# Kernel tuning notes

Hardware: AMD Instinct MI355X
Metric: run time of the kernel (lower is better)

Reference implementation:

```python
import jax, jax.numpy as jnp
import numpy as np
from jax import lax

EPS = 1e-5
K = 32  # k_neighbor

def conv1(x, w):
    # x: [B, Cin, L], w: [Cout, Cin] (1x1 conv, no bias)
    return jnp.einsum('bcl,oc->bol', x, w)

def bn(x, g, b):
    # BatchNorm1d in training mode: batch statistics over (batch, length)
    m = jnp.mean(x, axis=(0, 2), keepdims=True)
    v = jnp.var(x, axis=(0, 2), keepdims=True)
    return g[None, :, None] * (x - m) / jnp.sqrt(v + EPS) + b[None, :, None]

def res_block(x, w1, g1, b1, w2, g2, b2):
    h = jax.nn.gelu(bn(conv1(x, w1), g1, b1), approximate=False)
    h = bn(conv1(h, w2), g2, b2)
    return jax.nn.gelu(h + x, approximate=False)

def extraction(x, conv_w, bn_g, bn_b, fw, fg, fb):
    # conv_w: [n_blocks, 2, C, C]; bn_g/bn_b: [n_blocks, 2, C]
    for i in range(conv_w.shape[0]):
        x = res_block(x, conv_w[i, 0], bn_g[i, 0], bn_b[i, 0],
                      conv_w[i, 1], bn_g[i, 1], bn_b[i, 1])
    # TransformerBlock: ffn (conv+BN) with residual + GELU
    return jax.nn.gelu(x + bn(conv1(x, fw), fg, fb), approximate=False)

def setup_inputs() -> dict:
    key = jax.random.key(0)
    ks = jax.random.split(key, 16)
    B, N, S, C = 8, 4096, 1024, 128  # C = out_channel = 2*channel
    inp = {
        'xyz': jax.random.normal(ks[0], (B, N, 3), dtype=jnp.float32),
        'x': jax.random.normal(ks[1], (B, 64, N), dtype=jnp.float32),
        'fps_idx': jax.random.randint(ks[2], (B, S), 0, N, dtype=jnp.int64),
        'pre_conv_w': jax.random.normal(ks[3], (2, 2, C, C), dtype=jnp.float32) * 0.05,
        'pre_bn_g': jnp.ones((2, 2, C), jnp.float32),
        'pre_bn_b': jnp.zeros((2, 2, C), jnp.float32),
        'pre_ffn_w': jax.random.normal(ks[4], (C, C), dtype=jnp.float32) * 0.05,
        'pre_ffn_g': jnp.ones((C,), jnp.float32),
        'pre_ffn_b': jnp.zeros((C,), jnp.float32),
        'pos_conv_w': jax.random.normal(ks[5], (2, 2, C, C), dtype=jnp.float32) * 0.05,
        'pos_bn_g': jnp.ones((2, 2, C), jnp.float32),
        'pos_bn_b': jnp.zeros((2, 2, C), jnp.float32),
        'pos_ffn_w': jax.random.normal(ks[6], (C, C), dtype=jnp.float32) * 0.05,
        'pos_ffn_g': jnp.ones((C,), jnp.float32),
        'pos_ffn_b': jnp.zeros((C,), jnp.float32),
    }
    return inp

def reference(xyz, x, fps_idx,
              pre_conv_w, pre_bn_g, pre_bn_b, pre_ffn_w, pre_ffn_g, pre_ffn_b,
              pos_conv_w, pos_bn_g, pos_bn_b, pos_ffn_w, pos_ffn_g, pos_ffn_b):
    B, N, _ = xyz.shape
    S = fps_idx.shape[1]
    points = jnp.swapaxes(x, 1, 2)  # [B, N, d]
    d = points.shape[-1]

    # --- LocalGrouper ---
    new_xyz = jnp.take_along_axis(xyz, fps_idx[:, :, None], axis=1)      # [B, S, 3]
    new_pts = jnp.take_along_axis(points, fps_idx[:, :, None], axis=1)  # [B, S, d]

    # squared distances [B, S, N]
    sqr = (jnp.sum(new_xyz ** 2, -1)[:, :, None]
           + jnp.sum(xyz ** 2, -1)[:, None, :]
           - 2.0 * jnp.einsum('bsc,bnc->bsn', new_xyz, xyz))
    idx = lax.top_k(-sqr, K)[1]  # [B, S, K] smallest distances

    grouped = jnp.take_along_axis(points, idx.reshape(B, S * K)[:, :, None],
                                  axis=1).reshape(B, S, K, d)
    center = new_pts[:, :, None, :]  # [B, S, 1, d]
    feat = jnp.concatenate([grouped - center,
                            jnp.broadcast_to(center, grouped.shape)], axis=-1)  # [B,S,K,2d]

    C = 2 * d
    # --- PreExtraction: [B,S,K,C] -> [B*S, C, K] -> maxpool -> [B, C, S] ---
    y = jnp.swapaxes(feat, 2, 3).reshape(B * S, C, K)
    y = extraction(y, pre_conv_w, pre_bn_g, pre_bn_b, pre_ffn_w, pre_ffn_g, pre_ffn_b)
    y = jnp.max(y, axis=-1).reshape(B, S, C)
    y = jnp.swapaxes(y, 1, 2)  # [B, C, S]

    # --- PosExtraction ---
    y = extraction(y, pos_conv_w, pos_bn_g, pos_bn_b, pos_ffn_w, pos_ffn_g, pos_ffn_b)
    return (new_xyz, y)
```

## Files before the change

kernel.cpp:

```cpp
#include <hip/hip_runtime.h>
#include <math.h>

typedef unsigned short ushort_t;
typedef unsigned long long u64;
typedef unsigned int uint32;

#define B_ 8
#define N_ 4096
#define S_ 1024
#define K_ 32
#define C_ 128
#define NCOL1 (B_*S_*K_)
#define NCOL2 (B_*S_)
#define EPS_ 1e-5f

typedef ushort_t us8 __attribute__((ext_vector_type(8)));
typedef short s16x8 __attribute__((ext_vector_type(8)));
typedef float f32x4 __attribute__((ext_vector_type(4)));

__device__ __forceinline__ float bf2f(ushort_t u){ return __uint_as_float(((uint32)u)<<16); }
__device__ __forceinline__ ushort_t f2bf(float f){
    uint32 x = __float_as_uint(f);
    return (ushort_t)((x + 0x7FFFu + ((x>>16)&1u)) >> 16);
}
__device__ __forceinline__ float gelu_f(float v){
    float az = fabsf(v)*0.70710678118654752f;
    float t  = __builtin_amdgcn_rcpf(fmaf(0.3275911f, az, 1.0f));
    float p  = fmaf(fmaf(fmaf(fmaf(1.061405429f, t, -1.453152027f), t, 1.421413741f), t,
                   -0.284496736f), t, 0.254829592f)*t;
    float e  = __expf(-az*az);
    float er = fmaf(-p, e, 1.0f);
    float s  = (v < 0.0f) ? -er : er;
    return 0.5f*v*(1.0f+s);
}
__device__ __forceinline__ u64 shfl_xor_u64(u64 v, int m){
    int lo = __shfl_xor((int)(v & 0xFFFFFFFFull), m, 64);
    int hi = __shfl_xor((int)(v >> 32), m, 64);
    return (((u64)(uint32)hi) << 32) | (uint32)lo;
}
__device__ __forceinline__ void gl_lds16(const char* gp, char* lp){
    __builtin_amdgcn_global_load_lds((const __attribute__((address_space(1))) void*)gp,
                                     (__attribute__((address_space(3))) void*)lp, 16, 0, 0);
}

__global__ __launch_bounds__(256) void transpose_kernel(const float* __restrict__ x, ushort_t* __restrict__ xTb){
    __shared__ float t[64][65];
    int b  = blockIdx.x >> 6;
    int n0 = (blockIdx.x & 63) * 64;
    int tx = threadIdx.x & 63, ty = threadIdx.x >> 6;
    #pragma unroll
    for (int i=0;i<16;i++){
        int c = i*4 + ty;
        t[c][tx] = x[((long)(b*64 + c))*N_ + n0 + tx];
    }
    __syncthreads();
    #pragma unroll
    for (int i=0;i<16;i++){
        int n = i*4 + ty;
        xTb[((long)(b*N_ + n0 + n))*64 + tx] = f2bf(t[tx][n]);
    }
}

__global__ __launch_bounds__(256) void knn_kernel(const float* __restrict__ xyz, const int* __restrict__ fps,
                                                  int* __restrict__ idxg, float* __restrict__ newxyz){
    __shared__ uint32 hist[4096];
    __shared__ u64    cand[1024];
    __shared__ u64    out_keys[64];
    __shared__ uint32 csum[256];
    __shared__ uint32 wtot[4];
    __shared__ uint32 shv[8];
    __shared__ u64    wred[4];
    __shared__ u64    winner;

    int tid = threadIdx.x;
    int wv = tid >> 6, l = tid & 63;
    int bs = blockIdx.x;
    int b  = bs >> 10;
    int qi = fps[bs];
    const float* qb = xyz + ((long)b*N_ + qi)*3;
    float qx = qb[0], qy = qb[1], qz = qb[2];
    if (tid < 3) newxyz[(long)bs*3 + tid] = qb[tid];
    const float* xb = xyz + (long)b*N_*3;

    for (int i=tid;i<1024;i+=256) hist[i]=0;
    if (tid < 8) shv[tid]=0;
    __syncthreads();

    uint32 dbits[16];
    #pragma unroll
    for (int i=0;i<16;i++){
        int n = i*256 + tid;
        float dx = xb[n*3+0]-qx, dy = xb[n*3+1]-qy, dz = xb[n*3+2]-qz;
        float d = dx*dx + dy*dy + dz*dz;
        dbits[i] = __float_as_uint(d);
        atomicAdd(&hist[dbits[i]>>21], 1u);
    }
    __syncthreads();

    {
        uint32 h4[4]; uint32 csumv=0;
        #pragma unroll
        for (int i=0;i<4;i++){ h4[i]=hist[tid*4+i]; csumv+=h4[i]; }
        uint32 sc = csumv;
        #pragma unroll
        for (int off=1; off<64; off<<=1){ uint32 o=__shfl_up(sc,off,64); if (l>=off) sc+=o; }
        if (l==63) wtot[wv]=sc;
        csum[tid]=sc;
        __syncthreads();
        uint32 base=0;
        for (int w2=0; w2<wv; w2++) base += wtot[w2];
        uint32 cum = base + csum[tid] - csumv;
        #pragma unroll
        for (int i=0;i<4;i++){
            if (cum <= 31u && 31u < cum + h4[i]){ shv[0]=(uint32)(tid*4+i); shv[1]=cum; }
            cum += h4[i];
        }
    }
    __syncthreads();
    uint32 b1 = shv[0], cl1 = shv[1];

    for (int i=tid;i<4096;i+=256) hist[i]=0;
    __syncthreads();
    #pragma unroll
    for (int i=0;i<16;i++){
        uint32 u = dbits[i];
        if ((u>>21)==b1) atomicAdd(&hist[(u>>9)&0xFFFu], 1u);
    }
    __syncthreads();

    uint32 r2 = 31u - cl1;
    {
        uint32 h[16]; uint32 csumv=0;
        #pragma unroll
        for (int i=0;i<16;i++){ h[i]=hist[tid*16+i]; csumv += h[i]; }
        uint32 sc = csumv;
        #pragma unroll
        for (int off=1; off<64; off<<=1){ uint32 o=__shfl_up(sc,off,64); if (l>=off) sc+=o; }
        if (l==63) wtot[wv]=sc;
        csum[tid]=sc;
        __syncthreads();
        uint32 base=0;
        for (int w2=0; w2<wv; w2++) base += wtot[w2];
        uint32 cum = base + csum[tid] - csumv;
        #pragma unroll
        for (int i=0;i<16;i++){
            if (cum <= r2 && r2 < cum + h[i]){ shv[2]=(uint32)(tid*16+i); shv[3]=cum; }
            cum += h[i];
        }
    }
    __syncthreads();
    uint32 b2 = shv[2], cl2 = shv[3];
    uint32 nless = cl1 + cl2;

    #pragma unroll
    for (int i=0;i<16;i++){
        uint32 u = dbits[i];
        int n = i*256 + tid;
        uint32 bb1 = u >> 21;
        if (bb1 > b1) continue;
        u64 key = (((u64)u)<<32) | (uint32)n;
        if (bb1 < b1){
            uint32 p = atomicAdd(&shv[4],1u); out_keys[p] = key;
        } else {
            uint32 bb2 = (u>>9)&0xFFFu;
            if (bb2 < b2){ uint32 p = atomicAdd(&shv[4],1u); out_keys[p] = key; }
            else if (bb2 == b2){ uint32 p = atomicAdd(&shv[5],1u); if (p < 1024u) cand[p] = key; }
        }
    }
    __syncthreads();

    if (shv[5] > 1024u){
        uint32 alive = 0xFFFFu;
        for (int r=0;r<K_;r++){
            u64 lmin = ~0ull;
            #pragma unroll
            for (int i=0;i<16;i++){
                u64 k = (((u64)dbits[i])<<32) | (uint32)(i*256+tid);
                if (((alive>>i)&1u) && k < lmin) lmin = k;
            }
            #pragma unroll
            for (int off=32; off>=1; off>>=1){
                u64 o = shfl_xor_u64(lmin, off);
                if (o < lmin) lmin = o;
            }
            if (l == 0) wred[wv] = lmin;
            __syncthreads();
            if (tid == 0){
                u64 m = wred[0];
                if (wred[1]<m) m=wred[1];
                if (wred[2]<m) m=wred[2];
                if (wred[3]<m) m=wred[3];
                winner = m;
                idxg[(long)bs*K_ + r] = (int)(m & 0xFFFFFFFFull);
            }
            __syncthreads();
            u64 w = winner;
            #pragma unroll
            for (int i=0;i<16;i++){
                u64 k = (((u64)dbits[i])<<32) | (uint32)(i*256+tid);
                if (k == w) alive &= ~(1u<<i);
            }
        }
    } else if (wv == 0){
        uint32 cb   = shv[5];
        uint32 need = 32u - nless;
        for (uint32 r=0; r<need; r++){
            u64 lmin = ~0ull;
            for (uint32 s=l; s<cb; s+=64){ u64 kk = cand[s]; if (kk < lmin) lmin = kk; }
            #pragma unroll
            for (int off=32; off>=1; off>>=1){
                u64 o = shfl_xor_u64(lmin, off);
                if (o < lmin) lmin = o;
            }
            for (uint32 s=l; s<cb; s+=64){ if (cand[s]==lmin) cand[s] = ~0ull; }
            if (l==0) out_keys[nless + r] = lmin;
        }
        u64 key = (l < 32) ? out_keys[l] : ~0ull;
        #pragma unroll
        for (uint32 k=2; k<=64; k<<=1){
            bool dir = ((l & k)==0);
            #pragma unroll
            for (uint32 j=k>>1; j>=1; j>>=1){
                u64 o = shfl_xor_u64(key, j);
                bool lower = ((l & j)==0);
                u64 mn = (key < o) ? key : o;
                u64 mx = (key < o) ? o : key;
                key = (lower == dir) ? mn : mx;
            }
        }
        if (l < 32) idxg[(long)bs*K_ + l] = (int)(key & 0xFFFFFFFFull);
    }
}

__global__ __launch_bounds__(256) void wcvt_kernel(const float* __restrict__ pcw, const float* __restrict__ pfw,
                                                   const float* __restrict__ qcw, const float* __restrict__ qfw,
                                                   ushort_t* __restrict__ Wb, ushort_t* __restrict__ UW,
                                                   ushort_t* __restrict__ VW){
    int i = blockIdx.x*256 + threadIdx.x;
    if (i < 163840){
        int mat = i >> 14;
        int r = i & 16383;
        float v;
        if (mat < 4)       v = pcw[i];
        else if (mat == 4) v = pfw[r];
        else if (mat < 9)  v = qcw[i - 5*16384];
        else               v = qfw[r];
        Wb[i] = f2bf(v);
    } else {
        int j = i - 163840;
        int jj = j & 8191;
        int oc = jj >> 6, c = jj & 63;
        if (j < 8192) UW[jj] = f2bf(pcw[oc*128 + c]);
        else          VW[jj] = f2bf(pcw[oc*128 + 64 + c] - pcw[oc*128 + c]);
    }
}

__global__ __launch_bounds__(256) void uv_gemm(const ushort_t* __restrict__ xTb, const int* __restrict__ fps,
                                               const ushort_t* __restrict__ UW, const ushort_t* __restrict__ VW,
                                               ushort_t* __restrict__ U, ushort_t* __restrict__ V2){
    int tid = threadIdx.x;
    int w = tid >> 6, l = tid & 63;
    int l15 = l & 15, l4 = l >> 4;
    bool isV = blockIdx.x >= 256;
    int base = (isV ? (int)(blockIdx.x - 256) : (int)blockIdx.x)*128 + w*32;
    const ushort_t* Wh = isV ? VW : UW;
    ushort_t* out = isV ? V2 : U;

    long xrow[2];
    #pragma unroll
    for (int n=0;n<2;n++){
        int r = base + n*16 + l15;
        if (isV){ int b = r >> 10; xrow[n] = ((long)(b<<12) + fps[r]); }
        else    { xrow[n] = r; }
    }
    f32x4 acc[8][2] = {};
    #pragma unroll
    for (int ks=0; ks<2; ks++){
        int kl = ks*32 + l4*8;
        s16x8 af[8];
        #pragma unroll
        for (int m=0;m<8;m++)
            af[m] = *(const s16x8*)(Wh + (m*16 + l15)*64 + kl);
        s16x8 bv[2];
        #pragma unroll
        for (int n=0;n<2;n++)
            bv[n] = *(const s16x8*)(xTb + xrow[n]*64 + kl);
        #pragma unroll
        for (int m=0;m<8;m++)
            #pragma unroll
            for (int n=0;n<2;n++)
                acc[m][n] = __builtin_amdgcn_mfma_f32_16x16x32_bf16(af[m], bv[n], acc[m][n], 0, 0, 0);
    }
    #pragma unroll
    for (int n=0;n<2;n++){
        long radr = (long)(base + n*16 + l15)*C_;
        #pragma unroll
        for (int m=0;m<8;m++){
            f32x4 a = acc[m][n];
            uint2 st;
            st.x = (((uint32)f2bf(a[1]))<<16) | f2bf(a[0]);
            st.y = (((uint32)f2bf(a[3]))<<16) | f2bf(a[2]);
            *(uint2*)(out + radr + m*16 + l4*4) = st;
        }
    }
}

template<int MODE>
__global__ __launch_bounds__(256) void conv_mfma(const ushort_t* in1, const ushort_t* in2, ushort_t* aux,
                                                 ushort_t* out, const ushort_t* __restrict__ Wb,
                                                 const float* __restrict__ scsh_g,
                                                 const ushort_t* __restrict__ U, const ushort_t* __restrict__ V2,
                                                 const ushort_t* __restrict__ xTb, const int* __restrict__ idxg,
                                                 const int* __restrict__ fps,
                                                 float* __restrict__ pb, int nb, float inv_cnt){
    __shared__ ushort_t inT[16384];
    __shared__ float ss[256];
    __shared__ float sL[4][128], qL[4][128];
    int tid = threadIdx.x;
    int w = tid >> 6, l = tid & 63;
    int l15 = l & 15, l4 = l >> 4;
    long col0 = ((long)blockIdx.x << 7) + ((long)w << 5);

    if (MODE != 3){
        const char* gt = (const char*)(in1 + (((long)blockIdx.x) << 7)*C_);
        char* lb = (char*)inT;
        #pragma unroll
        for (int i=0;i<8;i++){
            int p = i*4096 + w*1024 + l*16;
            int src = p ^ (((p>>8)&7)<<4);
            gl_lds16(gt + src, lb + i*4096 + w*1024);
        }
    }

    s16x8 a2[8];
    if (MODE == 2){
        #pragma unroll
        for (int t=0;t<8;t++){
            int n = t>>2, ks = t&3;
            a2[t] = *(const s16x8*)(in2 + (col0 + n*16 + l15)*C_ + ks*32 + l4*8);
        }
    }
    if (MODE == 4){
        int bs = (int)(col0 >> 5);
        int b  = bs >> 10;
        int cc = fps[bs];
        const ushort_t* crow = xTb + ((long)(b<<12) + cc)*64;
        s16x8 c0 = *(const s16x8*)(crow + l4*8);
        s16x8 c1 = *(const s16x8*)(crow + 32 + l4*8);
        #pragma unroll
        for (int n=0;n<2;n++){
            int nn = idxg[col0 + n*16 + l15];
            const ushort_t* prow = xTb + ((long)(b<<12) + nn)*64;
            s16x8 p0 = *(const s16x8*)(prow + l4*8);
            s16x8 p1 = *(const s16x8*)(prow + 32 + l4*8);
            s16x8 d0, d1;
            #pragma unroll
            for (int e=0;e<8;e++){
                d0[e] = (short)f2bf(bf2f((ushort_t)p0[e]) - bf2f((ushort_t)c0[e]));
                d1[e] = (short)f2bf(bf2f((ushort_t)p1[e]) - bf2f((ushort_t)c1[e]));
            }
            a2[n*4+0] = d0; a2[n*4+1] = d1; a2[n*4+2] = c0; a2[n*4+3] = c1;
        }
    }
    if (MODE == 1 || MODE == 2 || MODE == 4) ss[tid] = scsh_g[tid];
    __syncthreads();

    f32x4 acc[8][2] = {};
    if (MODE == 3){
        int bs = (int)(col0 >> 5);
        int b  = bs >> 10;
        const ushort_t* vrow = V2 + (long)bs*C_;
        #pragma unroll
        for (int n=0;n<2;n++){
            int nn = idxg[col0 + n*16 + l15];
            const ushort_t* urow = U + ((long)(b*4096) + nn)*C_;
            #pragma unroll
            for (int m=0;m<8;m++){
                int oc0 = m*16 + l4*4;
                uint2 uu = *(const uint2*)(urow + oc0);
                uint2 vv = *(const uint2*)(vrow + oc0);
                acc[m][n][0] = bf2f((ushort_t)(uu.x & 0xFFFFu)) + bf2f((ushort_t)(vv.x & 0xFFFFu));
                acc[m][n][1] = bf2f((ushort_t)(uu.x >> 16))     + bf2f((ushort_t)(vv.x >> 16));
                acc[m][n][2] = bf2f((ushort_t)(uu.y & 0xFFFFu)) + bf2f((ushort_t)(vv.y & 0xFFFFu));
                acc[m][n][3] = bf2f((ushort_t)(uu.y >> 16))     + bf2f((ushort_t)(vv.y >> 16));
            }
        }
    } else {
        char* lb = (char*)inT;
        #pragma unroll
        for (int ks=0; ks<4; ks++){
            int kl = ks*32 + l4*8;
            s16x8 af[8];
            #pragma unroll
            for (int m=0;m<8;m++)
                af[m] = *(const s16x8*)(Wb + (m*16 + l15)*C_ + kl);
            s16x8 bv[2];
            int qsv[2];
            #pragma unroll
            for (int n=0;n<2;n++){
                int q = (w*32 + n*16 + l15)*256 + ks*64 + l4*16;
                qsv[n] = q ^ (((q>>8)&7)<<4);
                bv[n] = *(const s16x8*)(lb + qsv[n]);
            }
            if (MODE != 0){
                float sc[8], sh[8];
                const float4* sp = (const float4*)(&ss[kl*2]);
                float4 s0 = sp[0], s1 = sp[1], s2 = sp[2], s3 = sp[3];
                sc[0]=s0.x; sh[0]=s0.y; sc[1]=s0.z; sh[1]=s0.w;
                sc[2]=s1.x; sh[2]=s1.y; sc[3]=s1.z; sh[3]=s1.w;
                sc[4]=s2.x; sh[4]=s2.y; sc[5]=s2.z; sh[5]=s2.w;
                sc[6]=s3.x; sh[6]=s3.y; sc[7]=s3.z; sh[7]=s3.w;
                #pragma unroll
                for (int n=0;n<2;n++){
                    s16x8 v = bv[n];
                    if (MODE == 1){
                        #pragma unroll
                        for (int e=0;e<8;e++){
                            float f = gelu_f(fmaf(bf2f((ushort_t)v[e]), sc[e], sh[e]));
                            v[e] = (short)f2bf(f);
                        }
                    } else {
                        s16x8 a = a2[n*4+ks];
                        #pragma unroll
                        for (int e=0;e<8;e++){
                            float f = gelu_f(fmaf(bf2f((ushort_t)v[e]), sc[e], sh[e]) + bf2f((ushort_t)a[e]));
                            v[e] = (short)f2bf(f);
                        }
                    }
                    bv[n] = v;
                    if (MODE == 2 || MODE == 4)
                        *(s16x8*)(lb + qsv[n]) = v;
                }
            }
            #pragma unroll
            for (int m=0;m<8;m++)
                #pragma unroll
                for (int n=0;n<2;n++)
                    acc[m][n] = __builtin_amdgcn_mfma_f32_16x16x32_bf16(af[m], bv[n], acc[m][n], 0, 0, 0);
        }
    }

    if (MODE == 2 || MODE == 4){
        __syncthreads();
        char* auxb = (char*)aux + ((long)blockIdx.x << 15);
        const char* lb = (const char*)inT;
        #pragma unroll
        for (int i=0;i<8;i++){
            int lin = i*4096 + tid*16;
            int qs = lin ^ (((lin>>8)&7)<<4);
            *(f32x4*)(auxb + lin) = *(const f32x4*)(lb + qs);
        }
        __syncthreads();
    }

    {
        char* lb = (char*)inT;
        #pragma unroll
        for (int n=0;n<2;n++){
            #pragma unroll
            for (int m=0;m<8;m++){
                f32x4 a = acc[m][n];
                uint2 st;
                st.x = (((uint32)f2bf(a[1]))<<16) | f2bf(a[0]);
                st.y = (((uint32)f2bf(a[3]))<<16) | f2bf(a[2]);
                int q = (w*32 + n*16 + l15)*256 + (m*16 + l4*4)*2;
                int qs = q ^ (((q>>8)&7)<<4);
                *(uint2*)(lb + qs) = st;
            }
        }
        __syncthreads();
        char* outb = (char*)out + ((long)blockIdx.x << 15);
        const char* lb2 = (const char*)inT;
        #pragma unroll
        for (int i=0;i<8;i++){
            int lin = i*4096 + tid*16;
            int qs = lin ^ (((lin>>8)&7)<<4);
            *(f32x4*)(outb + lin) = *(const f32x4*)(lb2 + qs);
        }
    }

    #pragma unroll
    for (int m=0;m<8;m++){
        #pragma unroll
        for (int r=0;r<4;r++){
            float a0=acc[m][0][r], a1=acc[m][1][r];
            float s = a0+a1;
            float q = a0*a0+a1*a1;
            #pragma unroll
            for (int off=1; off<16; off<<=1){
                s += __shfl_xor(s, off, 64);
                q += __shfl_xor(q, off, 64);
            }
            if (l15 == 0){
                sL[w][m*16 + l4*4 + r] = s;
                qL[w][m*16 + l4*4 + r] = q;
            }
        }
    }
    __syncthreads();
    if (tid < 128){
        float s = sL[0][tid] + sL[1][tid] + sL[2][tid] + sL[3][tid];
        float q = qL[0][tid] + qL[1][tid] + qL[2][tid] + qL[3][tid];
        pb[(long)tid*nb + blockIdx.x]       = s;
        pb[(long)(128+tid)*nb + blockIdx.x] = q;
    }
}

__global__ __launch_bounds__(256) void reduce_fin_kernel(const float* __restrict__ pb, float* __restrict__ scsh,
                                                         const float* __restrict__ g, const float* __restrict__ bb,
                                                         float inv_cnt, int nb){
    int oc = blockIdx.x;
    float s=0.f, q=0.f;
    for (int b=threadIdx.x; b<nb; b+=256){
        s += pb[(long)oc*nb + b];
        q += pb[(long)(128+oc)*nb + b];
    }
    __shared__ float ls[256], lq[256];
    ls[threadIdx.x]=s; lq[threadIdx.x]=q;
    __syncthreads();
    #pragma unroll
    for (int st_=128; st_>0; st_>>=1){
        if (threadIdx.x < st_){ ls[threadIdx.x]+=ls[threadIdx.x+st_]; lq[threadIdx.x]+=lq[threadIdx.x+st_]; }
        __syncthreads();
    }
    if (threadIdx.x==0){
        float mean = ls[0]*inv_cnt;
        float var  = lq[0]*inv_cnt - mean*mean;
        float sc   = g[oc]*rsqrtf(var + EPS_);
        scsh[oc*2+0] = sc;
        scsh[oc*2+1] = bb[oc] - mean*sc;
    }
}

__global__ __launch_bounds__(256) void pool_kernel(const ushort_t* __restrict__ T, const ushort_t* __restrict__ X,
                                                   const float* __restrict__ scsh, ushort_t* __restrict__ A2){
    long p  = (long)blockIdx.x*256 + threadIdx.x;
    long bs = p >> 6;
    int  c0 = ((int)p & 63)*2;
    float sc0=scsh[c0*2], sh0=scsh[c0*2+1], sc1=scsh[c0*2+2], sh1=scsh[c0*2+3];
    const ushort_t* tb = T + (bs*K_)*(long)C_ + c0;
    const ushort_t* xv = X + (bs*K_)*(long)C_ + c0;
    float m0 = -1e30f, m1 = -1e30f;
    #pragma unroll 4
    for (int k=0;k<K_;k++){
        uint32 tv = *(const uint32*)(tb + (long)k*C_);
        uint32 av = *(const uint32*)(xv + (long)k*C_);
        float v0 = gelu_f(fmaf(bf2f((ushort_t)(tv & 0xFFFFu)), sc0, sh0) + bf2f((ushort_t)(av & 0xFFFFu)));
        float v1 = gelu_f(fmaf(bf2f((ushort_t)(tv >> 16)),     sc1, sh1) + bf2f((ushort_t)(av >> 16)));
        m0 = fmaxf(m0, v0);
        m1 = fmaxf(m1, v1);
    }
    uint32 o = (((uint32)f2bf(m1))<<16) | f2bf(m0);
    *(uint32*)(A2 + bs*C_ + c0) = o;
}

__global__ __launch_bounds__(256) void out2_kernel(const ushort_t* __restrict__ T, const ushort_t* __restrict__ X,
                                                   const float* __restrict__ scsh_g, float* __restrict__ y){
    __shared__ ushort_t Ts[16384];
    __shared__ ushort_t Xs[16384];
    __shared__ float ss[256];
    int tid = threadIdx.x, w = tid>>6, l = tid&63;
    int blk = blockIdx.x;

    {
        const char* gt = (const char*)(T + ((long)blk << 7)*C_);
        const char* gx = (const char*)(X + ((long)blk << 7)*C_);
        #pragma unroll
        for (int i=0;i<8;i++){
            int p = i*4096 + w*1024 + l*16;
            int src = p ^ (((p>>8)&7)<<4);
            gl_lds16(gt + src, (char*)Ts + i*4096 + w*1024);
            gl_lds16(gx + src, (char*)Xs + i*4096 + w*1024);
        }
    }
    ss[tid] = scsh_g[tid];
    __syncthreads();

    int b  = blk >> 3;
    int s0 = (blk & 7) * 128;
    int colL = tid & 127;
    int rep  = tid >> 7;
    #pragma unroll
    for (int cb=0; cb<8; cb++){
        int q  = colL*256 + rep*128 + cb*16;
        int qs = q ^ (((q>>8)&7)<<4);
        s16x8 tvv = *(const s16x8*)((char*)Ts + qs);
        s16x8 xvv = *(const s16x8*)((char*)Xs + qs);
        #pragma unroll
        for (int e=0;e<8;e++){
            int c = rep*64 + cb*8 + e;
            float f = gelu_f(fmaf(bf2f((ushort_t)tvv[e]), ss[c*2], ss[c*2+1]) + bf2f((ushort_t)xvv[e]));
            y[((long)(b*C_ + c))*S_ + s0 + colL] = f;
        }
    }
}

extern "C" void kernel_launch(void* const* d_in, const int* in_sizes, int n_in,
                              void* d_out, int out_size, void* d_ws, size_t ws_size,
                              hipStream_t stream){
    const float* xyz        = (const float*)d_in[0];
    const float* x          = (const float*)d_in[1];
    const int*   fps        = (const int*)d_in[2];
    const float* pre_conv_w = (const float*)d_in[3];
    const float* pre_bn_g   = (const float*)d_in[4];
    const float* pre_bn_b   = (const float*)d_in[5];
    const float* pre_ffn_w  = (const float*)d_in[6];
    const float* pre_ffn_g  = (const float*)d_in[7];
    const float* pre_ffn_b  = (const float*)d_in[8];
    const float* pos_conv_w = (const float*)d_in[9];
    const float* pos_bn_g   = (const float*)d_in[10];
    const float* pos_bn_b   = (const float*)d_in[11];
    const float* pos_ffn_w  = (const float*)d_in[12];
    const float* pos_ffn_g  = (const float*)d_in[13];
    const float* pos_ffn_b  = (const float*)d_in[14];

    float* out_xyz = (float*)d_out;
    float* out_y   = (float*)d_out + (long)B_*S_*3;

    char* ws = (char*)d_ws;
    float*    scsh = (float*)(ws + 0);
    float*    pbE  = (float*)(ws + 10240);
    ushort_t* Wb   = (ushort_t*)(ws + 337920);
    ushort_t* UW   = (ushort_t*)(ws + 665600);
    ushort_t* VW   = (ushort_t*)(ws + 681984);
    int*      idx  = (int*)(ws + 698368);
    ushort_t* xTb  = (ushort_t*)(ws + 1746944);
    ushort_t* A2   = (ushort_t*)(ws + 5941248);
    float*    pb1  = (float*)(ws + 8038400);
    ushort_t* C2   = (ushort_t*)(ws + 8038400);
    ushort_t* Cb   = (ushort_t*)(ws + 10135552);
    ushort_t* X    = (ushort_t*)(ws + 77244416);
    ushort_t* U    = (ushort_t*)(ws + 77244416);
    ushort_t* V2   = (ushort_t*)(ws + 85633024);
    (void)in_sizes; (void)n_in; (void)out_size; (void)ws_size;

    const float inv1 = 1.0f/(float)NCOL1, inv2 = 1.0f/(float)NCOL2;
    const ushort_t* Wp = Wb;
    const ushort_t* Wq = Wb + 5*C_*C_;
    const int nb = 2048;

    wcvt_kernel<<<704,256,0,stream>>>(pre_conv_w, pre_ffn_w, pos_conv_w, pos_ffn_w, Wb, UW, VW);
    transpose_kernel<<<B_*(N_/64),256,0,stream>>>(x, xTb);
    knn_kernel<<<B_*S_,256,0,stream>>>(xyz, fps, idx, out_xyz);
    uv_gemm<<<320,256,0,stream>>>(xTb, fps, UW, VW, U, V2);

    {
        const float* G[5]  = {pre_bn_g, pre_bn_g+C_, pre_bn_g+2*C_, pre_bn_g+3*C_, pre_ffn_g};
        const float* Bv[5] = {pre_bn_b, pre_bn_b+C_, pre_bn_b+2*C_, pre_bn_b+3*C_, pre_ffn_b};
        conv_mfma<3><<<nb,256,0,stream>>>(nullptr, nullptr, nullptr, Cb, nullptr, nullptr,
                                          U, V2, nullptr, idx, fps, pb1, nb, inv1);
        reduce_fin_kernel<<<128,256,0,stream>>>(pb1, scsh+0*256, G[0], Bv[0], inv1, nb);
        conv_mfma<1><<<nb,256,0,stream>>>(Cb, nullptr, nullptr, Cb, Wp+1*C_*C_, scsh+0*256,
                                          nullptr, nullptr, nullptr, nullptr, nullptr, pb1, nb, inv1);
        reduce_fin_kernel<<<128,256,0,stream>>>(pb1, scsh+1*256, G[1], Bv[1], inv1, nb);
        conv_mfma<4><<<nb,256,0,stream>>>(Cb, nullptr, X, Cb, Wp+2*C_*C_, scsh+1*256,
                                          nullptr, nullptr, xTb, idx, fps, pb1, nb, inv1);
        reduce_fin_kernel<<<128,256,0,stream>>>(pb1, scsh+2*256, G[2], Bv[2], inv1, nb);
        conv_mfma<1><<<nb,256,0,stream>>>(Cb, nullptr, nullptr, Cb, Wp+3*C_*C_, scsh+2*256,
                                          nullptr, nullptr, nullptr, nullptr, nullptr, pb1, nb, inv1);
        reduce_fin_kernel<<<128,256,0,stream>>>(pb1, scsh+3*256, G[3], Bv[3], inv1, nb);
        conv_mfma<2><<<nb,256,0,stream>>>(Cb, X, X, Cb, Wp+4*C_*C_, scsh+3*256,
                                          nullptr, nullptr, nullptr, nullptr, nullptr, pb1, nb, inv1);
        reduce_fin_kernel<<<128,256,0,stream>>>(pb1, scsh+4*256, G[4], Bv[4], inv1, nb);
        pool_kernel<<<(NCOL2*64)/256,256,0,stream>>>(Cb, X, scsh+4*256, A2);
    }

    {
        const float* G[5]  = {pos_bn_g, pos_bn_g+C_, pos_bn_g+2*C_, pos_bn_g+3*C_, pos_ffn_g};
        const float* Bv[5] = {pos_bn_b, pos_bn_b+C_, pos_bn_b+2*C_, pos_bn_b+3*C_, pos_ffn_b};
        const int nb2 = 64;
        conv_mfma<0><<<nb2,256,0,stream>>>(A2, nullptr, nullptr, C2, Wq+0*C_*C_, nullptr,
                                           nullptr, nullptr, nullptr, nullptr, nullptr, pbE, nb2, inv2);
        reduce_fin_kernel<<<128,256,0,stream>>>(pbE, scsh+5*256, G[0], Bv[0], inv2, nb2);
        conv_mfma<1><<<nb2,256,0,stream>>>(C2, nullptr, nullptr, C2, Wq+1*C_*C_, scsh+5*256,
                                           nullptr, nullptr, nullptr, nullptr, nullptr, pbE, nb2, inv2);
        reduce_fin_kernel<<<128,256,0,stream>>>(pbE, scsh+6*256, G[1], Bv[1], inv2, nb2);
        conv_mfma<2><<<nb2,256,0,stream>>>(C2, A2, A2, C2, Wq+2*C_*C_, scsh+6*256,
                                           nullptr, nullptr, nullptr, nullptr, nullptr, pbE, nb2, inv2);
        reduce_fin_kernel<<<128,256,0,stream>>>(pbE, scsh+7*256, G[2], Bv[2], inv2, nb2);
        conv_mfma<1><<<nb2,256,0,stream>>>(C2, nullptr, nullptr, C2, Wq+3*C_*C_, scsh+7*256,
                                           nullptr, nullptr, nullptr, nullptr, nullptr, pbE, nb2, inv2);
        reduce_fin_kernel<<<128,256,0,stream>>>(pbE, scsh+8*256, G[3], Bv[3], inv2, nb2);
        conv_mfma<2><<<nb2,256,0,stream>>>(C2, A2, A2, C2, Wq+4*C_*C_, scsh+8*256,
                                           nullptr, nullptr, nullptr, nullptr, nullptr, pbE, nb2, inv2);
        reduce_fin_kernel<<<128,256,0,stream>>>(pbE, scsh+9*256, G[4], Bv[4], inv2, nb2);
        out2_kernel<<<64,256,0,stream>>>(C2, A2, scsh+9*256, out_y);
    }
}
```

Before: 583.5 us.

## Double-buffer conv tiles with async LDS prefetch and split gather-add kernel

Replaces the monolithic conv_mfma with conv_pipe. Each block now processes two 64-column tiles, prefetching the next tile into a second LDS buffer through global_load_lds while the current tile runs its MFMAs. Outputs and aux residuals are written straight from registers to global memory, dropping the LDS staging round-trip and its extra barriers, and BN stats are accumulated across tiles. The MODE 3 gather-add path moves into its own gadd_kernel. The trade-off is less parallelism per tile (16 columns per wave), scattered uint2 global stores, and a hard vmcnt(0) wait that may limit overlap.

```diff
diff --git a/kernel.cpp b/kernel.cpp
--- a/kernel.cpp
+++ b/kernel.cpp
@@ -14,7 +14,6 @@
 #define NCOL2 (B_*S_)
 #define EPS_ 1e-5f
 
-typedef ushort_t us8 __attribute__((ext_vector_type(8)));
 typedef short s16x8 __attribute__((ext_vector_type(8)));
 typedef float f32x4 __attribute__((ext_vector_type(4)));
 
@@ -42,6 +41,9 @@
     __builtin_amdgcn_global_load_lds((const __attribute__((address_space(1))) void*)gp,
                                      (__attribute__((address_space(3))) void*)lp, 16, 0, 0);
 }
+#define PIN_VMCNT0() do{ __builtin_amdgcn_sched_barrier(0); \
+                         asm volatile("s_waitcnt vmcnt(0)" ::: "memory"); \
+                         __builtin_amdgcn_sched_barrier(0); }while(0)
 
 __global__ __launch_bounds__(256) void transpose_kernel(const float* __restrict__ x, ushort_t* __restrict__ xTb){
     __shared__ float t[64][65];
@@ -305,88 +307,172 @@
     }
 }
 
-template<int MODE>
-__global__ __launch_bounds__(256) void conv_mfma(const ushort_t* in1, const ushort_t* in2, ushort_t* aux,
-                                                 ushort_t* out, const ushort_t* __restrict__ Wb,
-                                                 const float* __restrict__ scsh_g,
-                                                 const ushort_t* __restrict__ U, const ushort_t* __restrict__ V2,
-                                                 const ushort_t* __restrict__ xTb, const int* __restrict__ idxg,
-                                                 const int* __restrict__ fps,
-                                                 float* __restrict__ pb, int nb, float inv_cnt){
-    __shared__ ushort_t inT[16384];
+__global__ __launch_bounds__(256) void gadd_kernel(const ushort_t* __restrict__ U, const ushort_t* __restrict__ V2,
+                                                   const int* __restrict__ idxg, ushort_t* __restrict__ out,
+                                                   float* __restrict__ pb, int nb){
+    __shared__ float sL[4][128], qL[4][128];
+    int tid = threadIdx.x;
+    int w = tid >> 6, l = tid & 63;
+    int l15 = l & 15, l4 = l >> 4;
+    long col0 = ((long)blockIdx.x << 7) + ((long)w << 5);
+    int bs = (int)(col0 >> 5);
+    int b  = bs >> 10;
+    const ushort_t* vrow = V2 + (long)bs*C_;
+
+    f32x4 acc[8][2];
+    #pragma unroll
+    for (int n=0;n<2;n++){
+        int nn = idxg[col0 + n*16 + l15];
+        const ushort_t* urow = U + ((long)(b*4096) + nn)*C_;
+        #pragma unroll
+        for (int m=0;m<8;m++){
+            int oc0 = m*16 + l4*4;
+            uint2 uu = *(const uint2*)(urow + oc0);
+            uint2 vv = *(const uint2*)(vrow + oc0);
+            acc[m][n][0] = bf2f((ushort_t)(uu.x & 0xFFFFu)) + bf2f((ushort_t)(vv.x & 0xFFFFu));
+            acc[m][n][1] = bf2f((ushort_t)(uu.x >> 16))     + bf2f((ushort_t)(vv.x >> 16));
+            acc[m][n][2] = bf2f((ushort_t)(uu.y & 0xFFFFu)) + bf2f((ushort_t)(vv.y & 0xFFFFu));
+            acc[m][n][3] = bf2f((ushort_t)(uu.y >> 16))     + bf2f((ushort_t)(vv.y >> 16));
+        }
+    }
+    #pragma unroll
+    for (int n=0;n<2;n++){
+        long cadr = (col0 + n*16 + l15)*C_;
+        #pragma unroll
+        for (int m=0;m<8;m++){
+            f32x4 a = acc[m][n];
+            uint2 st;
+            st.x = (((uint32)f2bf(a[1]))<<16) | f2bf(a[0]);
+            st.y = (((uint32)f2bf(a[3]))<<16) | f2bf(a[2]);
+            *(uint2*)(out + cadr + m*16 + l4*4) = st;
+        }
+    }
+    #pragma unroll
+    for (int m=0;m<8;m++){
+        #pragma unroll
+        for (int r=0;r<4;r++){
+            float a0=acc[m][0][r], a1=acc[m][1][r];
+            float s = a0+a1;
+            float q = a0*a0+a1*a1;
+            #pragma unroll
+            for (int off=1; off<16; off<<=1){
+                s += __shfl_xor(s, off, 64);
+                q += __shfl_xor(q, off, 64);
+            }
+            if (l15 == 0){
+                sL[w][m*16 + l4*4 + r] = s;
+                qL[w][m*16 + l4*4 + r] = q;
+            }
+        }
+    }
+    __syncthreads();
+    if (tid < 128){
+        float s = sL[0][tid] + sL[1][tid] + sL[2][tid] + sL[3][tid];
+        float q = qL[0][tid] + qL[1][tid] + qL[2][tid] + qL[3][tid];
+        pb[(long)tid*nb + blockIdx.x]       = s;
+        pb[(long)(128+tid)*nb + blockIdx.x] = q;
+    }
+}
+
+template<int MODE, int NT>
+__global__ __launch_bounds__(256, 4) void conv_pipe(const ushort_t* in1, const ushort_t* in2, ushort_t* aux,
+        ushort_t* out, const ushort_t* __restrict__ Wb, const float* __restrict__ scsh_g,
+        const ushort_t* __restrict__ xTb, const int* __restrict__ idxg, const int* __restrict__ fps,
+        float* __restrict__ pb, int nb){
+    __shared__ ushort_t inT[2][8192];
     __shared__ float ss[256];
     __shared__ float sL[4][128], qL[4][128];
     int tid = threadIdx.x;
     int w = tid >> 6, l = tid & 63;
     int l15 = l & 15, l4 = l >> 4;
-    long col0 = ((long)blockIdx.x << 7) + ((long)w << 5);
-
-    if (MODE != 3){
-        const char* gt = (const char*)(in1 + (((long)blockIdx.x) << 7)*C_);
-        char* lb = (char*)inT;
-        #pragma unroll
-        for (int i=0;i<8;i++){
-            int p = i*4096 + w*1024 + l*16;
+    int G = gridDim.x;
+
+    sL[w][l] = 0.f; sL[w][64+l] = 0.f;
+    qL[w][l] = 0.f; qL[w][64+l] = 0.f;
+
+    {
+        const char* gt = (const char*)in1 + ((long)blockIdx.x << 14);
+        #pragma unroll
+        for (int i=0;i<4;i++){
+            int p = (w<<12) + (i<<10) + (l<<4);
             int src = p ^ (((p>>8)&7)<<4);
-            gl_lds16(gt + src, lb + i*4096 + w*1024);
-        }
-    }
-
-    s16x8 a2[8];
+            gl_lds16(gt + src, (char*)&inT[0][0] + (w<<12) + (i<<10));
+        }
+    }
+    s16x8 a2cur[4], a2nxt[4];
     if (MODE == 2){
-        #pragma unroll
-        for (int t=0;t<8;t++){
-            int n = t>>2, ks = t&3;
-            a2[t] = *(const s16x8*)(in2 + (col0 + n*16 + l15)*C_ + ks*32 + l4*8);
-        }
+        long c0 = ((long)blockIdx.x << 6) + (w<<4);
+        #pragma unroll
+        for (int ks=0;ks<4;ks++)
+            a2cur[ks] = *(const s16x8*)(in2 + (c0 + l15)*C_ + ks*32 + l4*8);
     }
     if (MODE == 4){
-        int bs = (int)(col0 >> 5);
+        long c0 = ((long)blockIdx.x << 6) + (w<<4);
+        int bs = (int)(c0 >> 5);
         int b  = bs >> 10;
         int cc = fps[bs];
         const ushort_t* crow = xTb + ((long)(b<<12) + cc)*64;
-        s16x8 c0 = *(const s16x8*)(crow + l4*8);
-        s16x8 c1 = *(const s16x8*)(crow + 32 + l4*8);
-        #pragma unroll
-        for (int n=0;n<2;n++){
-            int nn = idxg[col0 + n*16 + l15];
-            const ushort_t* prow = xTb + ((long)(b<<12) + nn)*64;
-            s16x8 p0 = *(const s16x8*)(prow + l4*8);
-            s16x8 p1 = *(const s16x8*)(prow + 32 + l4*8);
-            s16x8 d0, d1;
-            #pragma unroll
-            for (int e=0;e<8;e++){
-                d0[e] = (short)f2bf(bf2f((ushort_t)p0[e]) - bf2f((ushort_t)c0[e]));
-                d1[e] = (short)f2bf(bf2f((ushort_t)p1[e]) - bf2f((ushort_t)c1[e]));
-            }
-            a2[n*4+0] = d0; a2[n*4+1] = d1; a2[n*4+2] = c0; a2[n*4+3] = c1;
-        }
-    }
-    if (MODE == 1 || MODE == 2 || MODE == 4) ss[tid] = scsh_g[tid];
-    __syncthreads();
-
-    f32x4 acc[8][2] = {};
-    if (MODE == 3){
-        int bs = (int)(col0 >> 5);
-        int b  = bs >> 10;
-        const ushort_t* vrow = V2 + (long)bs*C_;
-        #pragma unroll
-        for (int n=0;n<2;n++){
-            int nn = idxg[col0 + n*16 + l15];
-            const ushort_t* urow = U + ((long)(b*4096) + nn)*C_;
-            #pragma unroll
-            for (int m=0;m<8;m++){
-                int oc0 = m*16 + l4*4;
-                uint2 uu = *(const uint2*)(urow + oc0);
-                uint2 vv = *(const uint2*)(vrow + oc0);
-                acc[m][n][0] = bf2f((ushort_t)(uu.x & 0xFFFFu)) + bf2f((ushort_t)(vv.x & 0xFFFFu));
-                acc[m][n][1] = bf2f((ushort_t)(uu.x >> 16))     + bf2f((ushort_t)(vv.x >> 16));
-                acc[m][n][2] = bf2f((ushort_t)(uu.y & 0xFFFFu)) + bf2f((ushort_t)(vv.y & 0xFFFFu));
-                acc[m][n][3] = bf2f((ushort_t)(uu.y >> 16))     + bf2f((ushort_t)(vv.y >> 16));
-            }
-        }
-    } else {
-        char* lb = (char*)inT;
+        s16x8 cv0 = *(const s16x8*)(crow + l4*8);
+        s16x8 cv1 = *(const s16x8*)(crow + 32 + l4*8);
+        int nn = idxg[c0 + l15];
+        const ushort_t* prow = xTb + ((long)(b<<12) + nn)*64;
+        s16x8 p0 = *(const s16x8*)(prow + l4*8);
+        s16x8 p1 = *(const s16x8*)(prow + 32 + l4*8);
+        s16x8 d0, d1;
+        #pragma unroll
+        for (int e=0;e<8;e++){
+            d0[e] = (short)f2bf(bf2f((ushort_t)p0[e]) - bf2f((ushort_t)cv0[e]));
+            d1[e] = (short)f2bf(bf2f((ushort_t)p1[e]) - bf2f((ushort_t)cv1[e]));
+        }
+        a2cur[0]=d0; a2cur[1]=d1; a2cur[2]=cv0; a2cur[3]=cv1;
+    }
+    if (MODE != 0) ss[tid] = scsh_g[tid];
+    __syncthreads();
+
+    #pragma unroll
+    for (int t=0; t<NT; t++){
+        long tile = (long)t*G + blockIdx.x;
+        long col0 = (tile << 6) + (w<<4);
+
+        if (t+1 < NT){
+            long tn = tile + G;
+            const char* gt = (const char*)in1 + (tn << 14);
+            #pragma unroll
+            for (int i=0;i<4;i++){
+                int p = (w<<12) + (i<<10) + (l<<4);
+                int src = p ^ (((p>>8)&7)<<4);
+                gl_lds16(gt + src, (char*)&inT[(t+1)&1][0] + (w<<12) + (i<<10));
+            }
+            if (MODE == 2){
+                long c1 = (tn << 6) + (w<<4);
+                #pragma unroll
+                for (int ks=0;ks<4;ks++)
+                    a2nxt[ks] = *(const s16x8*)(in2 + (c1 + l15)*C_ + ks*32 + l4*8);
+            }
+            if (MODE == 4){
+                long c1 = (tn << 6) + (w<<4);
+                int bs = (int)(c1 >> 5);
+                int b  = bs >> 10;
+                int cc = fps[bs];
+                const ushort_t* crow = xTb + ((long)(b<<12) + cc)*64;
+                s16x8 cv0 = *(const s16x8*)(crow + l4*8);
+                s16x8 cv1 = *(const s16x8*)(crow + 32 + l4*8);
+                int nn = idxg[c1 + l15];
+                const ushort_t* prow = xTb + ((long)(b<<12) + nn)*64;
+                s16x8 p0 = *(const s16x8*)(prow + l4*8);
+                s16x8 p1 = *(const s16x8*)(prow + 32 + l4*8);
+                s16x8 d0, d1;
+                #pragma unroll
+                for (int e=0;e<8;e++){
+                    d0[e] = (short)f2bf(bf2f((ushort_t)p0[e]) - bf2f((ushort_t)cv0[e]));
+                    d1[e] = (short)f2bf(bf2f((ushort_t)p1[e]) - bf2f((ushort_t)cv1[e]));
+                }
+                a2nxt[0]=d0; a2nxt[1]=d1; a2nxt[2]=cv0; a2nxt[3]=cv1;
+            }
+        }
+
+        const char* lb = (const char*)&inT[t&1][0];
+        f32x4 acc[8] = {};
         #pragma unroll
         for (int ks=0; ks<4; ks++){
             int kl = ks*32 + l4*8;
@@ -394,14 +480,9 @@
             #pragma unroll
             for (int m=0;m<8;m++)
                 af[m] = *(const s16x8*)(Wb + (m*16 + l15)*C_ + kl);
-            s16x8 bv[2];
-            int qsv[2];
-            #pragma unroll
-            for (int n=0;n<2;n++){
-                int q = (w*32 + n*16 + l15)*256 + ks*64 + l4*16;
-                qsv[n] = q ^ (((q>>8)&7)<<4);
-                bv[n] = *(const s16x8*)(lb + qsv[n]);
-            }
+            int q  = ((w<<4) + l15)*256 + ks*64 + (l4<<4);
+            int qs = q ^ (((q>>8)&7)<<4);
+            s16x8 v = *(const s16x8*)(lb + qs);
             if (MODE != 0){
                 float sc[8], sh[8];
                 const float4* sp = (const float4*)(&ss[kl*2]);
@@ -410,93 +491,67 @@
                 sc[2]=s1.x; sh[2]=s1.y; sc[3]=s1.z; sh[3]=s1.w;
                 sc[4]=s2.x; sh[4]=s2.y; sc[5]=s2.z; sh[5]=s2.w;
                 sc[6]=s3.x; sh[6]=s3.y; sc[7]=s3.z; sh[7]=s3.w;
-                #pragma unroll
-                for (int n=0;n<2;n++){
-                    s16x8 v = bv[n];
-                    if (MODE == 1){
-                        #pragma unroll
-                        for (int e=0;e<8;e++){
-                            float f = gelu_f(fmaf(bf2f((ushort_t)v[e]), sc[e], sh[e]));
-                            v[e] = (short)f2bf(f);
-                        }
-                    } else {
-                        s16x8 a = a2[n*4+ks];
-                        #pragma unroll
-                        for (int e=0;e<8;e++){
-                            float f = gelu_f(fmaf(bf2f((ushort_t)v[e]), sc[e], sh[e]) + bf2f((ushort_t)a[e]));
-                            v[e] = (short)f2bf(f);
-                        }
+                if (MODE == 1){
+                    #pragma unroll
+                    for (int e=0;e<8;e++){
+                        float f = gelu_f(fmaf(bf2f((ushort_t)v[e]), sc[e], sh[e]));
+                        v[e] = (short)f2bf(f);
                     }
-                    bv[n] = v;
-                    if (MODE == 2 || MODE == 4)
-                        *(s16x8*)(lb + qsv[n]) = v;
+                } else {
+                    s16x8 a = a2cur[ks];
+                    #pragma unroll
+                    for (int e=0;e<8;e++){
+                        float f = gelu_f(fmaf(bf2f((ushort_t)v[e]), sc[e], sh[e]) + bf2f((ushort_t)a[e]));
+                        v[e] = (short)f2bf(f);
+                    }
                 }
+                if (MODE == 2 || MODE == 4)
+                    *(s16x8*)(aux + (col0 + l15)*C_ + kl) = v;
             }
             #pragma unroll
             for (int m=0;m<8;m++)
-                #pragma unroll
-                for (int n=0;n<2;n++)
-                    acc[m][n] = __builtin_amdgcn_mfma_f32_16x16x32_bf16(af[m], bv[n], acc[m][n], 0, 0, 0);
-        }
-    }
-
-    if (MODE == 2 || MODE == 4){
-        __syncthreads();
-        char* auxb = (char*)aux + ((long)blockIdx.x << 15);
-        const char* lb = (const char*)inT;
-        #pragma unroll
-        for (int i=0;i<8;i++){
-            int lin = i*4096 + tid*16;
-            int qs = lin ^ (((lin>>8)&7)<<4);
-            *(f32x4*)(auxb + lin) = *(const f32x4*)(lb + qs);
-        }
-        __syncthreads();
-    }
-
-    {
-        char* lb = (char*)inT;
-        #pragma unroll
-        for (int n=0;n<2;n++){
+                acc[m] = __builtin_amdgcn_mfma_f32_16x16x32_bf16(af[m], v, acc[m], 0, 0, 0);
+        }
+
+        {
+            long cadr = (col0 + l15)*C_;
             #pragma unroll
             for (int m=0;m<8;m++){
-                f32x4 a = acc[m][n];
+                f32x4 a = acc[m];
                 uint2 st;
                 st.x = (((uint32)f2bf(a[1]))<<16) | f2bf(a[0]);
                 st.y = (((uint32)f2bf(a[3]))<<16) | f2bf(a[2]);
-                int q = (w*32 + n*16 + l15)*256 + (m*16 + l4*4)*2;
-                int qs = q ^ (((q>>8)&7)<<4);
-                *(uint2*)(lb + qs) = st;
-            }
-        }
-        __syncthreads();
-        char* outb = (char*)out + ((long)blockIdx.x << 15);
-        const char* lb2 = (const char*)inT;
-        #pragma unroll
-        for (int i=0;i<8;i++){
-            int lin = i*4096 + tid*16;
-            int qs = lin ^ (((lin>>8)&7)<<4);
-            *(f32x4*)(outb + lin) = *(const f32x4*)(lb2 + qs);
-        }
-    }
-
-    #pragma unroll
-    for (int m=0;m<8;m++){
-        #pragma unroll
-        for (int r=0;r<4;r++){
-            float a0=acc[m][0][r], a1=acc[m][1][r];
-            float s = a0+a1;
-            float q = a0*a0+a1*a1;
-            #pragma unroll
-            for (int off=1; off<16; off<<=1){
-                s += __shfl_xor(s, off, 64);
-                q += __shfl_xor(q, off, 64);
-            }
-            if (l15 == 0){
-                sL[w][m*16 + l4*4 + r] = s;
-                qL[w][m*16 + l4*4 + r] = q;
-            }
-        }
-    }
+                *(uint2*)(out + cadr + m*16 + l4*4) = st;
+            }
+        }
+
+        #pragma unroll
+        for (int m=0;m<8;m++){
+            #pragma unroll
+            for (int r=0;r<4;r++){
+                float s = acc[m][r];
+                float q = s*s;
+                #pragma unroll
+                for (int off=1; off<16; off<<=1){
+                    s += __shfl_xor(s, off, 64);
+                    q += __shfl_xor(q, off, 64);
+                }
+                if (l15 == 0){
+                    sL[w][m*16 + l4*4 + r] += s;
+                    qL[w][m*16 + l4*4 + r] += q;
+                }
+            }
+        }
+
+        if (t+1 < NT){
+            PIN_VMCNT0();
+            if (MODE == 2 || MODE == 4){
+                #pragma unroll
+                for (int ks=0;ks<4;ks++) a2cur[ks] = a2nxt[ks];
+            }
+        }
+    }
+
     __syncthreads();
     if (tid < 128){
         float s = sL[0][tid] + sL[1][tid] + sL[2][tid] + sL[3][tid];
@@ -601,16 +656,12 @@
     const float* xyz        = (const float*)d_in[0];
     const float* x          = (const float*)d_in[1];
     const int*   fps        = (const int*)d_in[2];
-    const float* pre_conv_w = (const float*)d_in[3];
     const float* pre_bn_g   = (const float*)d_in[4];
     const float* pre_bn_b   = (const float*)d_in[5];
-    const float* pre_ffn_w  = (const float*)d_in[6];
     const float* pre_ffn_g  = (const float*)d_in[7];
     const float* pre_ffn_b  = (const float*)d_in[8];
-    const float* pos_conv_w = (const float*)d_in[9];
     const float* pos_bn_g   = (const float*)d_in[10];
     const float* pos_bn_b   = (const float*)d_in[11];
-    const float* pos_ffn_w  = (const float*)d_in[12];
     const float* pos_ffn_g  = (const float*)d_in[13];
     const float* pos_ffn_b  = (const float*)d_in[14];
 
@@ -637,9 +688,11 @@
     const float inv1 = 1.0f/(float)NCOL1, inv2 = 1.0f/(float)NCOL2;
     const ushort_t* Wp = Wb;
     const ushort_t* Wq = Wb + 5*C_*C_;
-    const int nb = 2048;
-
-    wcvt_kernel<<<704,256,0,stream>>>(pre_conv_w, pre_ffn_w, pos_conv_w, pos_ffn_w, Wb, UW, VW);
+    const int G1 = 2048;
+    const int G2 = 64;
+
+    wcvt_kernel<<<704,256,0,stream>>>((const float*)d_in[3], (const float*)d_in[6],
+                                      (const float*)d_in[9], (const float*)d_in[12], Wb, UW, VW);
     transpose_kernel<<<B_*(N_/64),256,0,stream>>>(x, xTb);
     knn_kernel<<<B_*S_,256,0,stream>>>(xyz, fps, idx, out_xyz);
     uv_gemm<<<320,256,0,stream>>>(xTb, fps, UW, VW, U, V2);
@@ -647,43 +700,41 @@
     {
         const float* G[5]  = {pre_bn_g, pre_bn_g+C_, pre_bn_g+2*C_, pre_bn_g+3*C_, pre_ffn_g};
         const float* Bv[5] = {pre_bn_b, pre_bn_b+C_, pre_bn_b+2*C_, pre_bn_b+3*C_, pre_ffn_b};
-        conv_mfma<3><<<nb,256,0,stream>>>(nullptr, nullptr, nullptr, Cb, nullptr, nullptr,
-                                          U, V2, nullptr, idx, fps, pb1, nb, inv1);
-        reduce_fin_kernel<<<128,256,0,stream>>>(pb1, scsh+0*256, G[0], Bv[0], inv1, nb);
-        conv_mfma<1><<<nb,256,0,stream>>>(Cb, nullptr, nullptr, Cb, Wp+1*C_*C_, scsh+0*256,
-                                          nullptr, nullptr, nullptr, nullptr, nullptr, pb1, nb, inv1);
-        reduce_fin_kernel<<<128,256,0,stream>>>(pb1, scsh+1*256, G[1], Bv[1], inv1, nb);
-        conv_mfma<4><<<nb,256,0,stream>>>(Cb, nullptr, X, Cb, Wp+2*C_*C_, scsh+1*256,
-                                          nullptr, nullptr, xTb, idx, fps, pb1, nb, inv1);
-        reduce_fin_kernel<<<128,256,0,stream>>>(pb1, scsh+2*256, G[2], Bv[2], inv1, nb);
-        conv_mfma<1><<<nb,256,0,stream>>>(Cb, nullptr, nullptr, Cb, Wp+3*C_*C_, scsh+2*256,
-                                          nullptr, nullptr, nullptr, nullptr, nullptr, pb1, nb, inv1);
-        reduce_fin_kernel<<<128,256,0,stream>>>(pb1, scsh+3*256, G[3], Bv[3], inv1, nb);
-        conv_mfma<2><<<nb,256,0,stream>>>(Cb, X, X, Cb, Wp+4*C_*C_, scsh+3*256,
-                                          nullptr, nullptr, nullptr, nullptr, nullptr, pb1, nb, inv1);
-        reduce_fin_kernel<<<128,256,0,stream>>>(pb1, scsh+4*256, G[4], Bv[4], inv1, nb);
+        gadd_kernel<<<2048,256,0,stream>>>(U, V2, idx, Cb, pb1, 2048);
+        reduce_fin_kernel<<<128,256,0,stream>>>(pb1, scsh+0*256, G[0], Bv[0], inv1, 2048);
+        conv_pipe<1,2><<<G1,256,0,stream>>>(Cb, nullptr, nullptr, Cb, Wp+1*C_*C_, scsh+0*256,
+                                            nullptr, nullptr, nullptr, pb1, G1);
+        reduce_fin_kernel<<<128,256,0,stream>>>(pb1, scsh+1*256, G[1], Bv[1], inv1, G1);
+        conv_pipe<4,2><<<G1,256,0,stream>>>(Cb, nullptr, X, Cb, Wp+2*C_*C_, scsh+1*256,
+                                            xTb, idx, fps, pb1, G1);
+        reduce_fin_kernel<<<128,256,0,stream>>>(pb1, scsh+2*256, G[2], Bv[2], inv1, G1);
+        conv_pipe<1,2><<<G1,256,0,stream>>>(Cb, nullptr, nullptr, Cb, Wp+3*C_*C_, scsh+2*256,
+                                            nullptr, nullptr, nullptr, pb1, G1);
+        reduce_fin_kernel<<<128,256,0,stream>>>(pb1, scsh+3*256, G[3], Bv[3], inv1, G1);
+        conv_pipe<2,2><<<G1,256,0,stream>>>(Cb, X, X, Cb, Wp+4*C_*C_, scsh+3*256,
+                                            nullptr, nullptr, nullptr, pb1, G1);
+        reduce_fin_kernel<<<128,256,0,stream>>>(pb1, scsh+4*256, G[4], Bv[4], inv1, G1);
         pool_kernel<<<(NCOL2*64)/256,256,0,stream>>>(Cb, X, scsh+4*256, A2);
     }
 
     {
         const float* G[5]  = {pos_bn_g, pos_bn_g+C_, pos_bn_g+2*C_, pos_bn_g+3*C_, pos_ffn_g};
         const float* Bv[5] = {pos_bn_b, pos_bn_b+C_, pos_bn_b+2*C_, pos_bn_b+3*C_, pos_ffn_b};
-        const int nb2 = 64;
-        conv_mfma<0><<<nb2,256,0,stream>>>(A2, nullptr, nullptr, C2, Wq+0*C_*C_, nullptr,
-                                           nullptr, nullptr, nullptr, nullptr, nullptr, pbE, nb2, inv2);
-        reduce_fin_kernel<<<128,256,0,stream>>>(pbE, scsh+5*256, G[0], Bv[0], inv2, nb2);
-        conv_mfma<1><<<nb2,256,0,stream>>>(C2, nullptr, nullptr, C2, Wq+1*C_*C_, scsh+5*256,
-                                           nullptr, nullptr, nullptr, nullptr, nullptr, pbE, nb2, inv2);
-        reduce_fin_kernel<<<128,256,0,stream>>>(pbE, scsh+6*256, G[1], Bv[1], inv2, nb2);
-        conv_mfma<2><<<nb2,256,0,stream>>>(C2, A2, A2, C2, Wq+2*C_*C_, scsh+6*256,
-                                           nullptr, nullptr, nullptr, nullptr, nullptr, pbE, nb2, inv2);
-        reduce_fin_kernel<<<128,256,0,stream>>>(pbE, scsh+7*256, G[2], Bv[2], inv2, nb2);
-        conv_mfma<1><<<nb2,256,0,stream>>>(C2, nullptr, nullptr, C2, Wq+3*C_*C_, scsh+7*256,
-                                           nullptr, nullptr, nullptr, nullptr, nullptr, pbE, nb2, inv2);
-        reduce_fin_kernel<<<128,256,0,stream>>>(pbE, scsh+8*256, G[3], Bv[3], inv2, nb2);
-        conv_mfma<2><<<nb2,256,0,stream>>>(C2, A2, A2, C2, Wq+4*C_*C_, scsh+8*256,
-                                           nullptr, nullptr, nullptr, nullptr, nullptr, pbE, nb2, inv2);
-        reduce_fin_kernel<<<128,256,0,stream>>>(pbE, scsh+9*256, G[4], Bv[4], inv2, nb2);
+        conv_pipe<0,2><<<G2,256,0,stream>>>(A2, nullptr, nullptr, C2, Wq+0*C_*C_, nullptr,
+                                            nullptr, nullptr, nullptr, pbE, G2);
+        reduce_fin_kernel<<<128,256,0,stream>>>(pbE, scsh+5*256, G[0], Bv[0], inv2, G2);
+        conv_pipe<1,2><<<G2,256,0,stream>>>(C2, nullptr, nullptr, C2, Wq+1*C_*C_, scsh+5*256,
+                                            nullptr, nullptr, nullptr, pbE, G2);
+        reduce_fin_kernel<<<128,256,0,stream>>>(pbE, scsh+6*256, G[1], Bv[1], inv2, G2);
+        conv_pipe<2,2><<<G2,256,0,stream>>>(C2, A2, A2, C2, Wq+2*C_*C_, scsh+6*256,
+                                            nullptr, nullptr, nullptr, pbE, G2);
+        reduce_fin_kernel<<<128,256,0,stream>>>(pbE, scsh+7*256, G[2], Bv[2], inv2, G2);
+        conv_pipe<1,2><<<G2,256,0,stream>>>(C2, nullptr, nullptr, C2, Wq+3*C_*C_, scsh+7*256,
+                                            nullptr, nullptr, nullptr, pbE, G2);
+        reduce_fin_kernel<<<128,256,0,stream>>>(pbE, scsh+8*256, G[3], Bv[3], inv2, G2);
+        conv_pipe<2,2><<<G2,256,0,stream>>>(C2, A2, A2, C2, Wq+4*C_*C_, scsh+8*256,
+                                            nullptr, nullptr, nullptr, pbE, G2);
+        reduce_fin_kernel<<<128,256,0,stream>>>(pbE, scsh+9*256, G[4], Bv[4], inv2, G2);
         out2_kernel<<<64,256,0,stream>>>(C2, A2, scsh+9*256, out_y);
     }
 }
```

New measurement: 727.4 us. 1.25x slower.
